# Kernel optimization log

Hardware: AMD Instinct MI355X
Metric: run time of the kernel (lower is better)

## Reference

```python
import jax, jax.numpy as jnp
import numpy as np

B, N_TOKENS, D, K = 16, 4096, 256, 4096
COMMITMENT_COST = 0.25


def setup_inputs() -> dict:
    key = jax.random.key(0)
    k1, k2 = jax.random.split(key)
    x = jax.random.normal(k1, (B, N_TOKENS, D), dtype=jnp.float32)
    # nn.Embedding init uniform(-1/K, 1/K); scale is irrelevant to correctness,
    # use the same distribution for fidelity.
    codebook = jax.random.uniform(k2, (K, D), dtype=jnp.float32,
                                  minval=-1.0 / K, maxval=1.0 / K)
    return {"x": x, "codebook": codebook}


def reference(x, codebook):
    Bb, Nn, Dd = x.shape
    x_flat = x.reshape(-1, Dd)                                    # [BN, D]
    dist_sq = (jnp.sum(x_flat * x_flat, axis=1, keepdims=True)
               + jnp.sum(codebook * codebook, axis=1)
               - 2.0 * x_flat @ codebook.T)                       # [BN, K]
    dist_sq = jnp.maximum(dist_sq, 0.0)
    idx = jnp.argmin(dist_sq, axis=1)                             # [BN]
    q_flat = codebook[idx]                                        # [BN, D]
    q = q_flat.reshape(x.shape)

    x_sg = jax.lax.stop_gradient(x_flat)
    q_sg = jax.lax.stop_gradient(q_flat)
    codebook_loss = jnp.mean((q_flat - x_sg) ** 2, axis=-1).reshape(Bb, Nn)
    commit_loss = jnp.mean((x_flat - q_sg) ** 2, axis=-1).reshape(Bb, Nn)
    per_token_loss = codebook_loss + COMMITMENT_COST * commit_loss
    mean_vq_loss = jnp.mean(per_token_loss)

    q_st = x + jax.lax.stop_gradient(q - x)                       # straight-through

    counts = jnp.zeros((codebook.shape[0],), dtype=jnp.float32).at[idx].add(1.0)
    avg_probs = counts / x_flat.shape[0]
    perplexity = jnp.exp(-jnp.sum(avg_probs * jnp.log(avg_probs + 1e-10)))

    return q_st, mean_vq_loss, perplexity, idx
```

## Files before the change

kernel.cpp:

```cpp
#include <hip/hip_runtime.h>
#include <hip/hip_bf16.h>
#include <cstdint>
#include <cstddef>

#define D 256
#define NTOK 65536
#define KCODES 4096
#define Q_ELEMS (NTOK * D)
#define DELTA 3.0e-4f
#define CAP 24

typedef short bf16x8 __attribute__((ext_vector_type(8)));
typedef float f32x4 __attribute__((ext_vector_type(4)));
typedef unsigned short ushort8 __attribute__((ext_vector_type(8)));

__device__ __forceinline__ void gload_lds16(const float* g, float* l) {
  __builtin_amdgcn_global_load_lds(
      (const __attribute__((address_space(1))) void*)(g),
      (__attribute__((address_space(3))) void*)(l), 16, 0, 0);
}
__device__ __forceinline__ unsigned short f2bf(float f) {
  __hip_bfloat16 h = __float2bfloat16(f);
  unsigned short u;
  __builtin_memcpy(&u, &h, 2);
  return u;
}
__device__ __forceinline__ float bf2f(unsigned short u) {
  __hip_bfloat16 h;
  __builtin_memcpy(&h, &u, 2);
  return __bfloat162float(h);
}

__global__ __launch_bounds__(256) void ee_kernel(const float* __restrict__ cb,
                                                 float* __restrict__ se) {
  const int row = blockIdx.x * 4 + (threadIdx.x >> 6);
  const int lane = threadIdx.x & 63;
  const float4 v = reinterpret_cast<const float4*>(cb + (size_t)row * D)[lane];
  double s = (double)v.x * v.x + (double)v.y * v.y +
             (double)v.z * v.z + (double)v.w * v.w;
#pragma unroll
  for (int o = 32; o > 0; o >>= 1) s += __shfl_down(s, o, 64);
  if (lane == 0) se[row] = (float)s;
}

__global__ __launch_bounds__(256) void xx_kernel(const float* __restrict__ x,
                                                 float* __restrict__ sx) {
  const int row = blockIdx.x * 4 + (threadIdx.x >> 6);
  const int lane = threadIdx.x & 63;
  const float4 v = reinterpret_cast<const float4*>(x + (size_t)row * D)[lane];
  double s = (double)v.x * v.x + (double)v.y * v.y +
             (double)v.z * v.z + (double)v.w * v.w;
#pragma unroll
  for (int o = 32; o > 0; o >>= 1) s += __shfl_down(s, o, 64);
  if (lane == 0) sx[row] = (float)s;
}

__global__ __launch_bounds__(256) void pack_e_kernel(const float* __restrict__ cb,
                                                     unsigned short* __restrict__ bpack) {
  const int gid = blockIdx.x * 256 + threadIdx.x;
  const int c = gid >> 2;
  const int kt = gid & 3;
  const int row = c & 127;
  const int swz = (row & 7) << 3;
  unsigned short* dst = bpack + ((size_t)((c >> 7) * 4 + kt)) * 8192 + row * 64;
  const float* src = cb + (size_t)c * D + kt * 64;
#pragma unroll
  for (int j = 0; j < 8; ++j) {
    ushort8 o;
#pragma unroll
    for (int e = 0; e < 8; ++e) o[e] = f2bf(src[j * 8 + e]);
    *reinterpret_cast<ushort8*>(dst + ((j * 8) ^ swz)) = o;
  }
}

__global__ __launch_bounds__(256, 2) void screen3_kernel(
    const float* __restrict__ x, const unsigned short* __restrict__ bpack,
    const float* __restrict__ se, unsigned int* __restrict__ ccnt_g,
    unsigned int* __restrict__ cand_g, float* __restrict__ rm_g) {
  __shared__ __attribute__((aligned(16))) unsigned short bbuf[3][8192];
  __shared__ __attribute__((aligned(16))) unsigned short se_lds[KCODES];
  __shared__ unsigned int cand[128][CAP];
  __shared__ unsigned int ccnt[128];

  const int tid = threadIdx.x;
  const int lane = tid & 63;
  const int w = tid >> 6;
  const int l15 = lane & 15;
  const int kg = lane >> 4;
  const int tok0 = blockIdx.x * 128;

  if (tid < 128) ccnt[tid] = 0;
  {
    const float4* s4 = reinterpret_cast<const float4*>(se) + tid * 4;
    const float4 a = s4[0], b = s4[1], c = s4[2], d = s4[3];
    ushort8 o0, o1;
    o0[0] = f2bf(a.x); o0[1] = f2bf(a.y); o0[2] = f2bf(a.z); o0[3] = f2bf(a.w);
    o0[4] = f2bf(b.x); o0[5] = f2bf(b.y); o0[6] = f2bf(b.z); o0[7] = f2bf(b.w);
    o1[0] = f2bf(c.x); o1[1] = f2bf(c.y); o1[2] = f2bf(c.z); o1[3] = f2bf(c.w);
    o1[4] = f2bf(d.x); o1[5] = f2bf(d.y); o1[6] = f2bf(d.z); o1[7] = f2bf(d.w);
    *reinterpret_cast<ushort8*>(&se_lds[tid * 16]) = o0;
    *reinterpret_cast<ushort8*>(&se_lds[tid * 16 + 8]) = o1;
  }

  bf16x8 ah[2][8];
#pragma unroll
  for (int gi = 0; gi < 2; ++gi) {
    const int t = tok0 + w * 32 + gi * 16 + l15;
    const float* xp = x + (size_t)t * D;
#pragma unroll
    for (int ks = 0; ks < 8; ++ks) {
      const float4 v0 = *reinterpret_cast<const float4*>(xp + ks * 32 + kg * 8);
      const float4 v1 = *reinterpret_cast<const float4*>(xp + ks * 32 + kg * 8 + 4);
      const float xv[8] = {v0.x, v0.y, v0.z, v0.w, v1.x, v1.y, v1.z, v1.w};
      bf16x8 h;
#pragma unroll
      for (int e = 0; e < 8; ++e) h[e] = (short)f2bf(xv[e]);
      ah[gi][ks] = h;
    }
  }

  auto STAGE = [&](int u) {
    const char* s = (const char*)bpack + (size_t)u * 16384 + w * 4096 + lane * 16;
    char* d = (char*)&bbuf[u % 3][0] + w * 4096;
    gload_lds16((const float*)s, (float*)d);
    gload_lds16((const float*)(s + 1024), (float*)(d + 1024));
    gload_lds16((const float*)(s + 2048), (float*)(d + 2048));
    gload_lds16((const float*)(s + 3072), (float*)(d + 3072));
  };

  float rm[2][4];
#pragma unroll
  for (int fr = 0; fr < 2; ++fr)
#pragma unroll
    for (int q = 0; q < 4; ++q) rm[fr][q] = 3.4e38f;

  f32x4 acc[2][8];

  STAGE(0);
  STAGE(1);
  __syncthreads();

  for (int ct4 = 0; ct4 < 32; ++ct4) {
#pragma unroll
    for (int kt = 0; kt < 4; ++kt) {
      const int u = ct4 * 4 + kt;
      if (u + 2 < 128) STAGE(u + 2);
      if (kt == 0) {
#pragma unroll
        for (int fr = 0; fr < 2; ++fr)
#pragma unroll
          for (int fc = 0; fc < 8; ++fc) acc[fr][fc] = (f32x4){0.f, 0.f, 0.f, 0.f};
      }
      const unsigned short* bb = &bbuf[u % 3][0];
#pragma unroll
      for (int kh = 0; kh < 2; ++kh) {
        const int ks = kt * 2 + kh;
        bf16x8 bfrag[8];
#pragma unroll
        for (int fc = 0; fc < 8; ++fc) {
          const int row = fc * 16 + l15;
          const int off = row * 64 + ((kh * 32 + kg * 8) ^ ((row & 7) << 3));
          bfrag[fc] = *reinterpret_cast<const bf16x8*>(bb + off);
        }
#pragma unroll
        for (int fr = 0; fr < 2; ++fr)
#pragma unroll
          for (int fc = 0; fc < 8; ++fc)
            acc[fr][fc] = __builtin_amdgcn_mfma_f32_16x16x32_bf16(
                ah[fr][ks], bfrag[fc], acc[fr][fc], 0, 0, 0);
      }
      if (kt == 3) {
        float sef[8];
#pragma unroll
        for (int fc = 0; fc < 8; ++fc)
          sef[fc] = bf2f(se_lds[ct4 * 128 + fc * 16 + l15]);
#pragma unroll
        for (int fr = 0; fr < 2; ++fr)
#pragma unroll
          for (int q = 0; q < 4; ++q) {
            float m = fmaf(-2.0f, acc[fr][0][q], sef[0]);
#pragma unroll
            for (int fc = 1; fc < 8; ++fc)
              m = fminf(m, fmaf(-2.0f, acc[fr][fc][q], sef[fc]));
            m = fminf(m, __shfl_xor(m, 1, 64));
            m = fminf(m, __shfl_xor(m, 2, 64));
            m = fminf(m, __shfl_xor(m, 4, 64));
            m = fminf(m, __shfl_xor(m, 8, 64));
            rm[fr][q] = fminf(rm[fr][q], m);
            const float thr = rm[fr][q] + DELTA;
            const int tl = w * 32 + fr * 16 + kg * 4 + q;
#pragma unroll
            for (int fc = 0; fc < 8; ++fc) {
              const float s = fmaf(-2.0f, acc[fr][fc][q], sef[fc]);
              if (s <= thr) {
                const unsigned p = atomicAdd(&ccnt[tl], 1u);
                if (p < CAP)
                  cand[tl][p] = ((unsigned)f2bf(s) << 16) |
                                (unsigned)(ct4 * 128 + fc * 16 + l15);
              }
            }
          }
      }
      __syncthreads();
    }
  }

  if (tid < 128) ccnt_g[tok0 + tid] = ccnt[tid];
  if (l15 == 0) {
#pragma unroll
    for (int fr = 0; fr < 2; ++fr)
#pragma unroll
      for (int q = 0; q < 4; ++q)
        rm_g[tok0 + w * 32 + fr * 16 + kg * 4 + q] = rm[fr][q];
  }
  for (int j = tid; j < 128 * CAP; j += 256)
    cand_g[(size_t)tok0 * CAP + j] = cand[j / CAP][j % CAP];
}

__global__ __launch_bounds__(256) void rescore_kernel(
    const float* __restrict__ x, const float* __restrict__ cb,
    const float* __restrict__ se, const float* __restrict__ sx,
    const unsigned int* __restrict__ ccnt_g, const unsigned int* __restrict__ cand_g,
    const float* __restrict__ rm_g, int* __restrict__ idx_i,
    float* __restrict__ idxf_out, unsigned int* __restrict__ ovf_count,
    int* __restrict__ ovf_list) {
  const int t = blockIdx.x * 256 + threadIdx.x;
  const unsigned n = ccnt_g[t];
  if (n > CAP) {
    const unsigned p = atomicAdd(ovf_count, 1u);
    ovf_list[p] = t;
    return;
  }
  const float thr = rm_g[t] + DELTA;
  const float sxv = sx[t];
  const float4* xp = reinterpret_cast<const float4*>(x + (size_t)t * D);
  float bq = 3.4e38f;
  int bc = 0x7fffffff;
  for (unsigned k = 0; k < n; ++k) {
    const unsigned pk = cand_g[(size_t)t * CAP + k];
    if (bf2f((unsigned short)(pk >> 16)) > thr) continue;
    const int c = (int)(pk & 0xFFFFu);
    const float4* cp = reinterpret_cast<const float4*>(cb + (size_t)c * D);
    float acc = 0.0f;
#pragma unroll 8
    for (int d4 = 0; d4 < 64; ++d4) {
      const float4 xv = xp[d4];
      const float4 ev = cp[d4];
      acc = fmaf(xv.x, ev.x, acc);
      acc = fmaf(xv.y, ev.y, acc);
      acc = fmaf(xv.z, ev.z, acc);
      acc = fmaf(xv.w, ev.w, acc);
    }
    const float r = sxv + se[c];
    const float q = r - 2.0f * acc;
    if (q < bq || (q == bq && c < bc)) { bq = q; bc = c; }
  }
  idx_i[t] = bc;
  idxf_out[t] = (float)bc;
}

__global__ __launch_bounds__(256) void ovf_kernel(
    const float* __restrict__ x, const float* __restrict__ cb,
    const float* __restrict__ se, const float* __restrict__ sx,
    const unsigned int* __restrict__ ovf_count, const int* __restrict__ ovf_list,
    int* __restrict__ idx_i, float* __restrict__ idxf_out) {
  __shared__ float bvv[256];
  __shared__ int bii[256];
  const int tid = threadIdx.x;
  const unsigned cnt = *ovf_count;
  for (unsigned i = blockIdx.x; i < cnt; i += gridDim.x) {
    const int t = ovf_list[i];
    const float sxv = sx[t];
    const float4* xp = reinterpret_cast<const float4*>(x + (size_t)t * D);
    float bq = 3.4e38f;
    int bc = 0x7fffffff;
    for (int c = tid; c < KCODES; c += 256) {
      const float4* cp = reinterpret_cast<const float4*>(cb + (size_t)c * D);
      float acc = 0.0f;
#pragma unroll 8
      for (int d4 = 0; d4 < 64; ++d4) {
        const float4 xv = xp[d4];
        const float4 ev = cp[d4];
        acc = fmaf(xv.x, ev.x, acc);
        acc = fmaf(xv.y, ev.y, acc);
        acc = fmaf(xv.z, ev.z, acc);
        acc = fmaf(xv.w, ev.w, acc);
      }
      const float r = sxv + se[c];
      const float q = r - 2.0f * acc;
      if (q < bq || (q == bq && c < bc)) { bq = q; bc = c; }
    }
    bvv[tid] = bq;
    bii[tid] = bc;
    __syncthreads();
    for (int o = 128; o > 0; o >>= 1) {
      if (tid < o) {
        const float v2 = bvv[tid + o];
        const int c2 = bii[tid + o];
        if (v2 < bvv[tid] || (v2 == bvv[tid] && c2 < bii[tid])) {
          bvv[tid] = v2;
          bii[tid] = c2;
        }
      }
      __syncthreads();
    }
    if (tid == 0) {
      idx_i[t] = bii[0];
      idxf_out[t] = (float)bii[0];
    }
    __syncthreads();
  }
}

__global__ __launch_bounds__(256) void argmin_fb_kernel(const float* __restrict__ x,
                                                        const float* __restrict__ cb,
                                                        const float* __restrict__ se,
                                                        const float* __restrict__ sx,
                                                        int* __restrict__ idx_out,
                                                        float* __restrict__ idxf_out) {
  __shared__ __attribute__((aligned(16))) float xs[64 * 128];
  __shared__ __attribute__((aligned(16))) float es[64 * 128];
  const int tid = threadIdx.x;
  const int lane = tid & 63;
  const int w = tid >> 6;
  const int wt = w & 1;
  const int wc = w >> 1;
  const int tgl = lane & 7;
  const int cgl = lane >> 3;
  const int t0 = wt * 64 + tgl * 8;
  const int c0 = wc * 64 + cgl * 8;
  const int tok0 = blockIdx.x * 128;
  float sxf[8];
#pragma unroll
  for (int i = 0; i < 8; ++i) sxf[i] = sx[tok0 + t0 + i];
  float bv[8];
  int bi[8];
#pragma unroll
  for (int i = 0; i < 8; ++i) { bv[i] = 3.4e38f; bi[i] = 0; }
  for (int ct = 0; ct < KCODES / 128; ++ct) {
    float acc[8][8] = {};
    for (int kt = 0; kt < 4; ++kt) {
      __syncthreads();
      {
        const float* xsrc = x + (size_t)tok0 * D + kt * 64;
        const float* esrc = cb + (size_t)(ct * 128) * D + kt * 64;
#pragma unroll
        for (int p = 0; p < 8; ++p) {
          const int idx = p * 256 + tid;
          const int t = idx >> 4;
          const int c = idx & 15;
          const int colp = (t + 8 * (c >> 1)) & 127;
          const float4 xv = *reinterpret_cast<const float4*>(xsrc + (size_t)t * D + c * 4);
          float* xd = &xs[(c * 4) * 128 + colp];
          xd[0] = xv.x; xd[128] = xv.y; xd[256] = xv.z; xd[384] = xv.w;
          const float4 ev = *reinterpret_cast<const float4*>(esrc + (size_t)t * D + c * 4);
          float* ed = &es[(c * 4) * 128 + colp];
          ed[0] = ev.x; ed[128] = ev.y; ed[256] = ev.z; ed[384] = ev.w;
        }
      }
      __syncthreads();
      for (int kp = 0; kp < 8; ++kp) {
        const float* xb = &xs[(kp * 8) * 128 + ((t0 + 8 * kp) & 127)];
        const float* eb = &es[(kp * 8) * 128 + ((c0 + 8 * kp) & 127)];
#pragma unroll
        for (int k2 = 0; k2 < 8; ++k2) {
          const float4 xv0 = *reinterpret_cast<const float4*>(xb + k2 * 128);
          const float4 xv1 = *reinterpret_cast<const float4*>(xb + k2 * 128 + 4);
          const float4 ev0 = *reinterpret_cast<const float4*>(eb + k2 * 128);
          const float4 ev1 = *reinterpret_cast<const float4*>(eb + k2 * 128 + 4);
          const float xa[8] = {xv0.x, xv0.y, xv0.z, xv0.w, xv1.x, xv1.y, xv1.z, xv1.w};
          const float ea[8] = {ev0.x, ev0.y, ev0.z, ev0.w, ev1.x, ev1.y, ev1.z, ev1.w};
#pragma unroll
          for (int i = 0; i < 8; ++i)
#pragma unroll
            for (int j = 0; j < 8; ++j) acc[i][j] = fmaf(xa[i], ea[j], acc[i][j]);
        }
      }
    }
#pragma unroll
    for (int j = 0; j < 8; ++j) {
      const int cidx = ct * 128 + c0 + j;
      const float sef = se[cidx];
#pragma unroll
      for (int i = 0; i < 8; ++i) {
        const float r = sxf[i] + sef;
        const float s = r - 2.0f * acc[i][j];
        if (s < bv[i]) { bv[i] = s; bi[i] = cidx; }
      }
    }
  }
  __syncthreads();
  float* red_val = xs;
  int* red_idx = reinterpret_cast<int*>(xs + 128 * 17);
  const int g = wc * 8 + cgl;
#pragma unroll
  for (int i = 0; i < 8; ++i) {
    red_val[(t0 + i) * 17 + g] = bv[i];
    red_idx[(t0 + i) * 17 + g] = bi[i];
  }
  __syncthreads();
  if (tid < 128) {
    float v = red_val[tid * 17 + 0];
    int ix = red_idx[tid * 17 + 0];
#pragma unroll
    for (int gg = 1; gg < 16; ++gg) {
      const float vv = red_val[tid * 17 + gg];
      const int ii = red_idx[tid * 17 + gg];
      if (vv < v || (vv == v && ii < ix)) { v = vv; ix = ii; }
    }
    idx_out[tok0 + tid] = ix;
    idxf_out[tok0 + tid] = (float)ix;
  }
}

__global__ __launch_bounds__(256) void finalize_kernel(const float* __restrict__ x,
                                                       const float* __restrict__ cb,
                                                       const int* __restrict__ idx,
                                                       float* __restrict__ q_out,
                                                       unsigned int* __restrict__ counts,
                                                       double* __restrict__ partials) {
  __shared__ double tok_s[16];
  const int tid = threadIdx.x;
  const int lt = tid >> 4;
  const int ld = tid & 15;
  const int t = blockIdx.x * 16 + lt;
  const int id = idx[t];
  const float* xp = x + (size_t)t * D + ld * 16;
  const float* ep = cb + (size_t)id * D + ld * 16;
  float* qp = q_out + (size_t)t * D + ld * 16;
  float s = 0.0f;
#pragma unroll
  for (int c = 0; c < 4; ++c) {
    const float4 xv = reinterpret_cast<const float4*>(xp)[c];
    const float4 ev = reinterpret_cast<const float4*>(ep)[c];
    const float d0 = ev.x - xv.x, d1 = ev.y - xv.y;
    const float d2 = ev.z - xv.z, d3 = ev.w - xv.w;
    s = fmaf(d0, d0, s);
    s = fmaf(d1, d1, s);
    s = fmaf(d2, d2, s);
    s = fmaf(d3, d3, s);
    float4 qv;
    qv.x = xv.x + d0;
    qv.y = xv.y + d1;
    qv.z = xv.z + d2;
    qv.w = xv.w + d3;
    reinterpret_cast<float4*>(qp)[c] = qv;
  }
#pragma unroll
  for (int o = 8; o > 0; o >>= 1) s += __shfl_down(s, o, 16);
  if (ld == 0) {
    atomicAdd(&counts[id], 1u);
    tok_s[lt] = (double)s;
  }
  __syncthreads();
  if (tid == 0) {
    double bs = 0.0;
    for (int i = 0; i < 16; ++i) bs += tok_s[i];
    partials[blockIdx.x] = bs;
  }
}

__global__ __launch_bounds__(256) void final_kernel(const unsigned int* __restrict__ counts,
                                                    const double* __restrict__ partials,
                                                    float* __restrict__ loss_out,
                                                    float* __restrict__ perp_out) {
  __shared__ double sh[256];
  const int tid = threadIdx.x;
  double ls = 0.0;
  for (int i = tid; i < NTOK / 16; i += 256) ls += partials[i];
  sh[tid] = ls;
  __syncthreads();
#pragma unroll
  for (int o = 128; o > 0; o >>= 1) {
    if (tid < o) sh[tid] += sh[tid + o];
    __syncthreads();
  }
  if (tid == 0) *loss_out = (float)(sh[0] * (1.25 / (256.0 * 65536.0)));
  __syncthreads();
  double hs = 0.0;
  for (int i = tid; i < KCODES; i += 256) {
    const float p = (float)counts[i] / 65536.0f;
    hs += (double)(p * logf(p + 1e-10f));
  }
  sh[tid] = hs;
  __syncthreads();
#pragma unroll
  for (int o = 128; o > 0; o >>= 1) {
    if (tid < o) sh[tid] += sh[tid + o];
    __syncthreads();
  }
  if (tid == 0) *perp_out = expf((float)(-sh[0]));
}

extern "C" void kernel_launch(void* const* d_in, const int* in_sizes, int n_in,
                              void* d_out, int out_size, void* d_ws, size_t ws_size,
                              hipStream_t stream) {
  (void)in_sizes; (void)n_in; (void)out_size;
  const float* x = (const float*)d_in[0];
  const float* cb = (const float*)d_in[1];

  float* out = (float*)d_out;
  float* q_out = out;
  float* loss_out = out + (size_t)Q_ELEMS;
  float* perp_out = out + (size_t)Q_ELEMS + 1;
  float* idxf_out = out + (size_t)Q_ELEMS + 2;

  char* ws = (char*)d_ws;
  float* se = (float*)(ws + 0);
  unsigned int* counts = (unsigned int*)(ws + (16 << 10));
  double* partials = (double*)(ws + (32 << 10));
  int* idx_i = (int*)(ws + (128 << 10));
  float* sx = (float*)(ws + (384 << 10));
  unsigned int* ovf_count = (unsigned int*)(ws + (640 << 10));
  int* ovf_list = (int*)(ws + (644 << 10));
  unsigned int* ccnt_g = (unsigned int*)(ws + (1 << 20));
  float* rm_g = (float*)(ws + (3 << 19));
  unsigned int* cand_g = (unsigned int*)(ws + (2 << 20));
  unsigned short* bpack = (unsigned short*)(ws + (14 << 20));

  hipMemsetAsync(counts, 0, KCODES * sizeof(unsigned int), stream);
  hipMemsetAsync(ovf_count, 0, sizeof(unsigned int), stream);
  ee_kernel<<<KCODES / 4, 256, 0, stream>>>(cb, se);
  xx_kernel<<<NTOK / 4, 256, 0, stream>>>(x, sx);

  if (ws_size >= (size_t)20 * 1024 * 1024) {
    pack_e_kernel<<<64, 256, 0, stream>>>(cb, bpack);
    screen3_kernel<<<NTOK / 128, 256, 0, stream>>>(x, bpack, se, ccnt_g, cand_g,
                                                   rm_g);
    rescore_kernel<<<NTOK / 256, 256, 0, stream>>>(x, cb, se, sx, ccnt_g, cand_g,
                                                   rm_g, idx_i, idxf_out,
                                                   ovf_count, ovf_list);
    ovf_kernel<<<64, 256, 0, stream>>>(x, cb, se, sx, ovf_count, ovf_list,
                                       idx_i, idxf_out);
  } else {
    argmin_fb_kernel<<<NTOK / 128, 256, 0, stream>>>(x, cb, se, sx, idx_i, idxf_out);
  }
  finalize_kernel<<<NTOK / 16, 256, 0, stream>>>(x, cb, idx_i, q_out, counts, partials);
  final_kernel<<<1, 256, 0, stream>>>(counts, partials, loss_out, perp_out);
}
```

Measured before the change: 365.6 us.

## Load codebook fragments directly from global into registers, dropping LDS staging

The screening kernel no longer stages packed codebook tiles through a triple-buffered LDS ring with per-step block barriers. The codebook is now pre-packed in MFMA fragment order so each lane reads its bf16x8 fragments straight from global memory (L2-resident), double-buffered in registers. This removes the per-k-step __syncthreads and the LDS round trip. The separate x-norm kernel is also dropped; rescore and overflow compute the x norms inline. The trade-off is more global/L2 traffic per block and more register pressure from the two fragment buffers.

```diff
diff --git a/kernel.cpp b/kernel.cpp
--- a/kernel.cpp
+++ b/kernel.cpp
@@ -14,11 +14,6 @@
 typedef float f32x4 __attribute__((ext_vector_type(4)));
 typedef unsigned short ushort8 __attribute__((ext_vector_type(8)));
 
-__device__ __forceinline__ void gload_lds16(const float* g, float* l) {
-  __builtin_amdgcn_global_load_lds(
-      (const __attribute__((address_space(1))) void*)(g),
-      (__attribute__((address_space(3))) void*)(l), 16, 0, 0);
-}
 __device__ __forceinline__ unsigned short f2bf(float f) {
   __hip_bfloat16 h = __float2bfloat16(f);
   unsigned short u;
@@ -61,23 +56,27 @@
   const int c = gid >> 2;
   const int kt = gid & 3;
   const int row = c & 127;
-  const int swz = (row & 7) << 3;
-  unsigned short* dst = bpack + ((size_t)((c >> 7) * 4 + kt)) * 8192 + row * 64;
+  const int fc = row >> 4;
+  const int l15 = row & 15;
+  const int unit = (c >> 7) * 4 + kt;
   const float* src = cb + (size_t)c * D + kt * 64;
 #pragma unroll
-  for (int j = 0; j < 8; ++j) {
-    ushort8 o;
-#pragma unroll
-    for (int e = 0; e < 8; ++e) o[e] = f2bf(src[j * 8 + e]);
-    *reinterpret_cast<ushort8*>(dst + ((j * 8) ^ swz)) = o;
-  }
-}
-
-__global__ __launch_bounds__(256, 2) void screen3_kernel(
+  for (int kh = 0; kh < 2; ++kh)
+#pragma unroll
+    for (int kg = 0; kg < 4; ++kg) {
+      ushort8 o;
+#pragma unroll
+      for (int e = 0; e < 8; ++e) o[e] = f2bf(src[kh * 32 + kg * 8 + e]);
+      *reinterpret_cast<ushort8*>(
+          bpack + (size_t)unit * 8192 + (kh * 8 + fc) * 512 +
+          (kg * 16 + l15) * 8) = o;
+    }
+}
+
+__global__ __launch_bounds__(256, 2) void screeng_kernel(
     const float* __restrict__ x, const unsigned short* __restrict__ bpack,
     const float* __restrict__ se, unsigned int* __restrict__ ccnt_g,
     unsigned int* __restrict__ cand_g, float* __restrict__ rm_g) {
-  __shared__ __attribute__((aligned(16))) unsigned short bbuf[3][8192];
   __shared__ __attribute__((aligned(16))) unsigned short se_lds[KCODES];
   __shared__ unsigned int cand[128][CAP];
   __shared__ unsigned int ccnt[128];
@@ -101,6 +100,7 @@
     *reinterpret_cast<ushort8*>(&se_lds[tid * 16]) = o0;
     *reinterpret_cast<ushort8*>(&se_lds[tid * 16 + 8]) = o1;
   }
+  __syncthreads();
 
   bf16x8 ah[2][8];
 #pragma unroll
@@ -119,13 +119,11 @@
     }
   }
 
-  auto STAGE = [&](int u) {
-    const char* s = (const char*)bpack + (size_t)u * 16384 + w * 4096 + lane * 16;
-    char* d = (char*)&bbuf[u % 3][0] + w * 4096;
-    gload_lds16((const float*)s, (float*)d);
-    gload_lds16((const float*)(s + 1024), (float*)(d + 1024));
-    gload_lds16((const float*)(s + 2048), (float*)(d + 2048));
-    gload_lds16((const float*)(s + 3072), (float*)(d + 3072));
+  auto LOADKH = [&](bf16x8 (&dst)[8], int g) {
+    const unsigned short* ub = bpack + (size_t)g * 4096 + lane * 8;
+#pragma unroll
+    for (int fc = 0; fc < 8; ++fc)
+      dst[fc] = *reinterpret_cast<const bf16x8*>(ub + fc * 512);
   };
 
   float rm[2][4];
@@ -135,76 +133,72 @@
     for (int q = 0; q < 4; ++q) rm[fr][q] = 3.4e38f;
 
   f32x4 acc[2][8];
-
-  STAGE(0);
-  STAGE(1);
-  __syncthreads();
+  bf16x8 b0[8], b1[8];
+  LOADKH(b0, 0);
 
   for (int ct4 = 0; ct4 < 32; ++ct4) {
 #pragma unroll
-    for (int kt = 0; kt < 4; ++kt) {
-      const int u = ct4 * 4 + kt;
-      if (u + 2 < 128) STAGE(u + 2);
-      if (kt == 0) {
-#pragma unroll
-        for (int fr = 0; fr < 2; ++fr)
-#pragma unroll
-          for (int fc = 0; fc < 8; ++fc) acc[fr][fc] = (f32x4){0.f, 0.f, 0.f, 0.f};
-      }
-      const unsigned short* bb = &bbuf[u % 3][0];
-#pragma unroll
-      for (int kh = 0; kh < 2; ++kh) {
-        const int ks = kt * 2 + kh;
-        bf16x8 bfrag[8];
-#pragma unroll
-        for (int fc = 0; fc < 8; ++fc) {
-          const int row = fc * 16 + l15;
-          const int off = row * 64 + ((kh * 32 + kg * 8) ^ ((row & 7) << 3));
-          bfrag[fc] = *reinterpret_cast<const bf16x8*>(bb + off);
-        }
+    for (int fr = 0; fr < 2; ++fr)
+#pragma unroll
+      for (int fc = 0; fc < 8; ++fc) acc[fr][fc] = (f32x4){0.f, 0.f, 0.f, 0.f};
+#pragma unroll
+    for (int p = 0; p < 8; ++p) {
+      const int gn = ct4 * 8 + p + 1;
+      if ((p & 1) == 0) {
+        if (gn < 256) LOADKH(b1, gn);
 #pragma unroll
         for (int fr = 0; fr < 2; ++fr)
 #pragma unroll
           for (int fc = 0; fc < 8; ++fc)
             acc[fr][fc] = __builtin_amdgcn_mfma_f32_16x16x32_bf16(
-                ah[fr][ks], bfrag[fc], acc[fr][fc], 0, 0, 0);
+                ah[fr][p], b0[fc], acc[fr][fc], 0, 0, 0);
+      } else {
+        if (gn < 256) LOADKH(b0, gn);
+#pragma unroll
+        for (int fr = 0; fr < 2; ++fr)
+#pragma unroll
+          for (int fc = 0; fc < 8; ++fc)
+            acc[fr][fc] = __builtin_amdgcn_mfma_f32_16x16x32_bf16(
+                ah[fr][p], b1[fc], acc[fr][fc], 0, 0, 0);
       }
-      if (kt == 3) {
-        float sef[8];
-#pragma unroll
-        for (int fc = 0; fc < 8; ++fc)
-          sef[fc] = bf2f(se_lds[ct4 * 128 + fc * 16 + l15]);
-#pragma unroll
-        for (int fr = 0; fr < 2; ++fr)
-#pragma unroll
-          for (int q = 0; q < 4; ++q) {
-            float m = fmaf(-2.0f, acc[fr][0][q], sef[0]);
-#pragma unroll
-            for (int fc = 1; fc < 8; ++fc)
-              m = fminf(m, fmaf(-2.0f, acc[fr][fc][q], sef[fc]));
-            m = fminf(m, __shfl_xor(m, 1, 64));
-            m = fminf(m, __shfl_xor(m, 2, 64));
-            m = fminf(m, __shfl_xor(m, 4, 64));
-            m = fminf(m, __shfl_xor(m, 8, 64));
-            rm[fr][q] = fminf(rm[fr][q], m);
-            const float thr = rm[fr][q] + DELTA;
-            const int tl = w * 32 + fr * 16 + kg * 4 + q;
-#pragma unroll
-            for (int fc = 0; fc < 8; ++fc) {
-              const float s = fmaf(-2.0f, acc[fr][fc][q], sef[fc]);
-              if (s <= thr) {
-                const unsigned p = atomicAdd(&ccnt[tl], 1u);
-                if (p < CAP)
-                  cand[tl][p] = ((unsigned)f2bf(s) << 16) |
-                                (unsigned)(ct4 * 128 + fc * 16 + l15);
-              }
+    }
+    {
+      float sef[8];
+#pragma unroll
+      for (int fc = 0; fc < 8; ++fc)
+        sef[fc] = bf2f(se_lds[ct4 * 128 + fc * 16 + l15]);
+#pragma unroll
+      for (int fr = 0; fr < 2; ++fr)
+#pragma unroll
+        for (int q = 0; q < 4; ++q) {
+          float s8[8];
+#pragma unroll
+          for (int fc = 0; fc < 8; ++fc)
+            s8[fc] = fmaf(-2.0f, acc[fr][fc][q], sef[fc]);
+          float m = s8[0];
+#pragma unroll
+          for (int fc = 1; fc < 8; ++fc) m = fminf(m, s8[fc]);
+          m = fminf(m, __shfl_xor(m, 1, 64));
+          m = fminf(m, __shfl_xor(m, 2, 64));
+          m = fminf(m, __shfl_xor(m, 4, 64));
+          m = fminf(m, __shfl_xor(m, 8, 64));
+          rm[fr][q] = fminf(rm[fr][q], m);
+          const float thr = rm[fr][q] + DELTA;
+          const int tl = w * 32 + fr * 16 + kg * 4 + q;
+#pragma unroll
+          for (int fc = 0; fc < 8; ++fc) {
+            if (s8[fc] <= thr) {
+              const unsigned p2 = atomicAdd(&ccnt[tl], 1u);
+              if (p2 < CAP)
+                cand[tl][p2] = ((unsigned)f2bf(s8[fc]) << 16) |
+                               (unsigned)(ct4 * 128 + fc * 16 + l15);
             }
           }
-      }
-      __syncthreads();
-    }
-  }
-
+        }
+    }
+  }
+
+  __syncthreads();
   if (tid < 128) ccnt_g[tok0 + tid] = ccnt[tid];
   if (l15 == 0) {
 #pragma unroll
@@ -219,11 +213,10 @@
 
 __global__ __launch_bounds__(256) void rescore_kernel(
     const float* __restrict__ x, const float* __restrict__ cb,
-    const float* __restrict__ se, const float* __restrict__ sx,
-    const unsigned int* __restrict__ ccnt_g, const unsigned int* __restrict__ cand_g,
-    const float* __restrict__ rm_g, int* __restrict__ idx_i,
-    float* __restrict__ idxf_out, unsigned int* __restrict__ ovf_count,
-    int* __restrict__ ovf_list) {
+    const float* __restrict__ se, const unsigned int* __restrict__ ccnt_g,
+    const unsigned int* __restrict__ cand_g, const float* __restrict__ rm_g,
+    int* __restrict__ idx_i, float* __restrict__ idxf_out,
+    unsigned int* __restrict__ ovf_count, int* __restrict__ ovf_list) {
   const int t = blockIdx.x * 256 + threadIdx.x;
   const unsigned n = ccnt_g[t];
   if (n > CAP) {
@@ -231,9 +224,15 @@
     ovf_list[p] = t;
     return;
   }
+  const float4* xp = reinterpret_cast<const float4*>(x + (size_t)t * D);
+  double sxd = 0.0;
+  for (int d4 = 0; d4 < 64; ++d4) {
+    const float4 v = xp[d4];
+    sxd += (double)v.x * v.x + (double)v.y * v.y +
+           (double)v.z * v.z + (double)v.w * v.w;
+  }
+  const float sxv = (float)sxd;
   const float thr = rm_g[t] + DELTA;
-  const float sxv = sx[t];
-  const float4* xp = reinterpret_cast<const float4*>(x + (size_t)t * D);
   float bq = 3.4e38f;
   int bc = 0x7fffffff;
   for (unsigned k = 0; k < n; ++k) {
@@ -261,16 +260,25 @@
 
 __global__ __launch_bounds__(256) void ovf_kernel(
     const float* __restrict__ x, const float* __restrict__ cb,
-    const float* __restrict__ se, const float* __restrict__ sx,
-    const unsigned int* __restrict__ ovf_count, const int* __restrict__ ovf_list,
-    int* __restrict__ idx_i, float* __restrict__ idxf_out) {
+    const float* __restrict__ se, const unsigned int* __restrict__ ovf_count,
+    const int* __restrict__ ovf_list, int* __restrict__ idx_i,
+    float* __restrict__ idxf_out) {
   __shared__ float bvv[256];
   __shared__ int bii[256];
+  __shared__ double shd[256];
   const int tid = threadIdx.x;
   const unsigned cnt = *ovf_count;
   for (unsigned i = blockIdx.x; i < cnt; i += gridDim.x) {
     const int t = ovf_list[i];
-    const float sxv = sx[t];
+    const float xv1 = x[(size_t)t * D + tid];
+    shd[tid] = (double)xv1 * xv1;
+    __syncthreads();
+    for (int o = 128; o > 0; o >>= 1) {
+      if (tid < o) shd[tid] += shd[tid + o];
+      __syncthreads();
+    }
+    const float sxv = (float)shd[0];
+    __syncthreads();
     const float4* xp = reinterpret_cast<const float4*>(x + (size_t)t * D);
     float bq = 3.4e38f;
     int bc = 0x7fffffff;
@@ -516,23 +524,23 @@
   unsigned int* ccnt_g = (unsigned int*)(ws + (1 << 20));
   float* rm_g = (float*)(ws + (3 << 19));
   unsigned int* cand_g = (unsigned int*)(ws + (2 << 20));
-  unsigned short* bpack = (unsigned short*)(ws + (14 << 20));
+  unsigned short* bpack = (unsigned short*)(ws + (12 << 20));
 
   hipMemsetAsync(counts, 0, KCODES * sizeof(unsigned int), stream);
   hipMemsetAsync(ovf_count, 0, sizeof(unsigned int), stream);
   ee_kernel<<<KCODES / 4, 256, 0, stream>>>(cb, se);
-  xx_kernel<<<NTOK / 4, 256, 0, stream>>>(x, sx);
 
   if (ws_size >= (size_t)20 * 1024 * 1024) {
     pack_e_kernel<<<64, 256, 0, stream>>>(cb, bpack);
-    screen3_kernel<<<NTOK / 128, 256, 0, stream>>>(x, bpack, se, ccnt_g, cand_g,
+    screeng_kernel<<<NTOK / 128, 256, 0, stream>>>(x, bpack, se, ccnt_g, cand_g,
                                                    rm_g);
-    rescore_kernel<<<NTOK / 256, 256, 0, stream>>>(x, cb, se, sx, ccnt_g, cand_g,
+    rescore_kernel<<<NTOK / 256, 256, 0, stream>>>(x, cb, se, ccnt_g, cand_g,
                                                    rm_g, idx_i, idxf_out,
                                                    ovf_count, ovf_list);
-    ovf_kernel<<<64, 256, 0, stream>>>(x, cb, se, sx, ovf_count, ovf_list,
+    ovf_kernel<<<64, 256, 0, stream>>>(x, cb, se, ovf_count, ovf_list,
                                        idx_i, idxf_out);
   } else {
+    xx_kernel<<<NTOK / 4, 256, 0, stream>>>(x, sx);
     argmin_fb_kernel<<<NTOK / 128, 256, 0, stream>>>(x, cb, se, sx, idx_i, idxf_out);
   }
   finalize_kernel<<<NTOK / 16, 256, 0, stream>>>(x, cb, idx_i, q_out, counts, partials);
```

After: 444.4 us. 1.22x slower.

## Relax screen pipeline barriers with vmcnt waits and fold x-norm into rescore

Applied to the files above, without the earlier changes.

The screening kernel's per-tile __syncthreads is replaced by explicit s_waitcnt vmcnt(4) plus a raw s_barrier, so the prefetch of the next staged codebook tile can stay in flight across the barrier instead of draining all outstanding loads. The separate xx_kernel pass that computed per-token squared norms is dropped on the main path. Rescore and overflow kernels now compute the norm inline in double precision, which re-reads x per token but saves a launch and a full pass over x. The hand-written wait counts depend on the exact number of global_load_lds ops per stage, so getting them wrong would risk reading LDS before it is filled.

```diff
diff --git a/kernel.cpp b/kernel.cpp
--- a/kernel.cpp
+++ b/kernel.cpp
@@ -73,7 +73,7 @@
   }
 }
 
-__global__ __launch_bounds__(256, 2) void screen3_kernel(
+__global__ __launch_bounds__(256, 2) void screen5_kernel(
     const float* __restrict__ x, const unsigned short* __restrict__ bpack,
     const float* __restrict__ se, unsigned int* __restrict__ ccnt_g,
     unsigned int* __restrict__ cand_g, float* __restrict__ rm_g) {
@@ -136,9 +136,13 @@
 
   f32x4 acc[2][8];
 
+  __builtin_amdgcn_sched_barrier(0);
+  asm volatile("s_waitcnt vmcnt(0)" ::: "memory");
   STAGE(0);
   STAGE(1);
-  __syncthreads();
+  asm volatile("s_waitcnt vmcnt(4) lgkmcnt(0)" ::: "memory");
+  __builtin_amdgcn_s_barrier();
+  __builtin_amdgcn_sched_barrier(0);
 
   for (int ct4 = 0; ct4 < 32; ++ct4) {
 #pragma unroll
@@ -201,10 +205,16 @@
             }
           }
       }
-      __syncthreads();
-    }
-  }
-
+      if (u != 127) {
+        if (u != 126) asm volatile("s_waitcnt vmcnt(4)" ::: "memory");
+        else          asm volatile("s_waitcnt vmcnt(0)" ::: "memory");
+        __builtin_amdgcn_s_barrier();
+        __builtin_amdgcn_sched_barrier(0);
+      }
+    }
+  }
+
+  __syncthreads();
   if (tid < 128) ccnt_g[tok0 + tid] = ccnt[tid];
   if (l15 == 0) {
 #pragma unroll
@@ -219,11 +229,10 @@
 
 __global__ __launch_bounds__(256) void rescore_kernel(
     const float* __restrict__ x, const float* __restrict__ cb,
-    const float* __restrict__ se, const float* __restrict__ sx,
-    const unsigned int* __restrict__ ccnt_g, const unsigned int* __restrict__ cand_g,
-    const float* __restrict__ rm_g, int* __restrict__ idx_i,
-    float* __restrict__ idxf_out, unsigned int* __restrict__ ovf_count,
-    int* __restrict__ ovf_list) {
+    const float* __restrict__ se, const unsigned int* __restrict__ ccnt_g,
+    const unsigned int* __restrict__ cand_g, const float* __restrict__ rm_g,
+    int* __restrict__ idx_i, float* __restrict__ idxf_out,
+    unsigned int* __restrict__ ovf_count, int* __restrict__ ovf_list) {
   const int t = blockIdx.x * 256 + threadIdx.x;
   const unsigned n = ccnt_g[t];
   if (n > CAP) {
@@ -231,9 +240,15 @@
     ovf_list[p] = t;
     return;
   }
+  const float4* xp = reinterpret_cast<const float4*>(x + (size_t)t * D);
+  double sxd = 0.0;
+  for (int d4 = 0; d4 < 64; ++d4) {
+    const float4 v = xp[d4];
+    sxd += (double)v.x * v.x + (double)v.y * v.y +
+           (double)v.z * v.z + (double)v.w * v.w;
+  }
+  const float sxv = (float)sxd;
   const float thr = rm_g[t] + DELTA;
-  const float sxv = sx[t];
-  const float4* xp = reinterpret_cast<const float4*>(x + (size_t)t * D);
   float bq = 3.4e38f;
   int bc = 0x7fffffff;
   for (unsigned k = 0; k < n; ++k) {
@@ -261,16 +276,25 @@
 
 __global__ __launch_bounds__(256) void ovf_kernel(
     const float* __restrict__ x, const float* __restrict__ cb,
-    const float* __restrict__ se, const float* __restrict__ sx,
-    const unsigned int* __restrict__ ovf_count, const int* __restrict__ ovf_list,
-    int* __restrict__ idx_i, float* __restrict__ idxf_out) {
+    const float* __restrict__ se, const unsigned int* __restrict__ ovf_count,
+    const int* __restrict__ ovf_list, int* __restrict__ idx_i,
+    float* __restrict__ idxf_out) {
   __shared__ float bvv[256];
   __shared__ int bii[256];
+  __shared__ double shd[256];
   const int tid = threadIdx.x;
   const unsigned cnt = *ovf_count;
   for (unsigned i = blockIdx.x; i < cnt; i += gridDim.x) {
     const int t = ovf_list[i];
-    const float sxv = sx[t];
+    const float xv1 = x[(size_t)t * D + tid];
+    shd[tid] = (double)xv1 * xv1;
+    __syncthreads();
+    for (int o = 128; o > 0; o >>= 1) {
+      if (tid < o) shd[tid] += shd[tid + o];
+      __syncthreads();
+    }
+    const float sxv = (float)shd[0];
+    __syncthreads();
     const float4* xp = reinterpret_cast<const float4*>(x + (size_t)t * D);
     float bq = 3.4e38f;
     int bc = 0x7fffffff;
@@ -516,23 +540,23 @@
   unsigned int* ccnt_g = (unsigned int*)(ws + (1 << 20));
   float* rm_g = (float*)(ws + (3 << 19));
   unsigned int* cand_g = (unsigned int*)(ws + (2 << 20));
-  unsigned short* bpack = (unsigned short*)(ws + (14 << 20));
+  unsigned short* bpack = (unsigned short*)(ws + (12 << 20));
 
   hipMemsetAsync(counts, 0, KCODES * sizeof(unsigned int), stream);
   hipMemsetAsync(ovf_count, 0, sizeof(unsigned int), stream);
   ee_kernel<<<KCODES / 4, 256, 0, stream>>>(cb, se);
-  xx_kernel<<<NTOK / 4, 256, 0, stream>>>(x, sx);
 
   if (ws_size >= (size_t)20 * 1024 * 1024) {
     pack_e_kernel<<<64, 256, 0, stream>>>(cb, bpack);
-    screen3_kernel<<<NTOK / 128, 256, 0, stream>>>(x, bpack, se, ccnt_g, cand_g,
+    screen5_kernel<<<NTOK / 128, 256, 0, stream>>>(x, bpack, se, ccnt_g, cand_g,
                                                    rm_g);
-    rescore_kernel<<<NTOK / 256, 256, 0, stream>>>(x, cb, se, sx, ccnt_g, cand_g,
+    rescore_kernel<<<NTOK / 256, 256, 0, stream>>>(x, cb, se, ccnt_g, cand_g,
                                                    rm_g, idx_i, idxf_out,
                                                    ovf_count, ovf_list);
-    ovf_kernel<<<64, 256, 0, stream>>>(x, cb, se, sx, ovf_count, ovf_list,
+    ovf_kernel<<<64, 256, 0, stream>>>(x, cb, se, ovf_count, ovf_list,
                                        idx_i, idxf_out);
   } else {
+    xx_kernel<<<NTOK / 4, 256, 0, stream>>>(x, sx);
     argmin_fb_kernel<<<NTOK / 128, 256, 0, stream>>>(x, cb, se, sx, idx_i, idxf_out);
   }
   finalize_kernel<<<NTOK / 16, 256, 0, stream>>>(x, cb, idx_i, q_out, counts, partials);
```

Result: faster. 358.1 us (-2.1%).
